# Optimization experiments

Measured on AMD Instinct MI355X. Metric: run time of the kernel, lower is better.

Reference implementation:

```python
import jax, jax.numpy as jnp
import numpy as np

T, D, H, O = 1048576, 64, 128, 32  # tokens, input_size, expert hidden, expert output_size


def setup_inputs() -> dict:
    key = jax.random.key(0)
    ks = jax.random.split(key, 11)
    s = 0.02
    return {
        "x": jax.random.normal(ks[0], (T, D), dtype=jnp.float32),
        "topk_idx": jax.random.randint(ks[1], (T, 2), 0, 2),
        "weights": jax.random.uniform(ks[2], (T, 2), dtype=jnp.float32),
        # expert 0: MLP D -> H -> O
        "W0a": jax.random.normal(ks[3], (D, H), dtype=jnp.float32) * s,
        "b0a": jnp.zeros((H,), dtype=jnp.float32),
        "W0b": jax.random.normal(ks[4], (H, O), dtype=jnp.float32) * s,
        "b0b": jnp.zeros((O,), dtype=jnp.float32),
        # expert 1: MLP (D + O) -> H -> O  (memory-enhanced input)
        "W1a": jax.random.normal(ks[5], (D + O, H), dtype=jnp.float32) * s,
        "b1a": jnp.zeros((H,), dtype=jnp.float32),
        "W1b": jax.random.normal(ks[6], (H, O), dtype=jnp.float32) * s,
        "b1b": jnp.zeros((O,), dtype=jnp.float32),
    }


def reference(x, topk_idx, weights, W0a, b0a, W0b, b0b, W1a, b1a, W1b, b1b):
    mask0 = (topk_idx == 0).any(axis=1)  # [T]
    mask1 = (topk_idx == 1).any(axis=1)  # [T]

    # expert 0 output, zero where not routed (matches zeros buffer + masked scatter)
    e0 = jnp.maximum(x @ W0a + b0a, 0.0) @ W0b + b0b      # [T, O]
    out0 = jnp.where(mask0[:, None], e0, 0.0)

    # last_valid_fill: forward-fill last valid row index (invalid -> 0, then cummax)
    t = jnp.arange(T)
    idx = jax.lax.cummax(jnp.where(mask0, t, 0))           # [T] int
    filled = out0[idx]                                     # [T, O] gather rows

    # expert 1 on [x, last_valid_out0], zero where not routed
    x1 = jnp.concatenate([x, filled], axis=1)              # [T, D+O]
    e1 = jnp.maximum(x1 @ W1a + b1a, 0.0) @ W1b + b1b      # [T, O]
    out1 = jnp.where(mask1[:, None], e1, 0.0)

    w = weights[:, :1]                                     # [T, 1]
    return w * out0 + (1.0 - w) * out1
```

## Files before the change

kernel.cpp:

```cpp
#include <hip/hip_runtime.h>
#include <hip/hip_bf16.h>

#define TROWS 1048576
#define RPB   256
#define NCHUNK (TROWS / RPB)
#define LSTRIDE 36

typedef float f32x4  __attribute__((ext_vector_type(4)));
typedef short bf16x8 __attribute__((ext_vector_type(8)));
typedef short bf16x4 __attribute__((ext_vector_type(4)));

#define MFMA(a, b, c) __builtin_amdgcn_mfma_f32_16x16x32_bf16(a, b, c, 0, 0, 0)

__device__ __forceinline__ short f2bf(float v) {
    __hip_bfloat16 b = __float2bfloat16(v);
    return __builtin_bit_cast(short, b);
}
__device__ __forceinline__ float bf2f(short s) {
    unsigned u = ((unsigned)(unsigned short)s) << 16;
    return __builtin_bit_cast(float, u);
}

__global__ __launch_bounds__(64) void prep_kernel(
    const float* __restrict__ W0a, const float* __restrict__ W0b,
    const float* __restrict__ W1a, const float* __restrict__ W1b,
    bf16x8* __restrict__ frag)
{
    const int fid = blockIdx.x, l = threadIdx.x, c = l & 15, g = l >> 4;
    const float* W; int N, ks, nt;
    if (fid < 16)      { W = W0a; N = 128; ks = fid >> 3;        nt = fid & 7; }
    else if (fid < 24) { W = W0b; N = 32;  ks = (fid - 16) >> 1; nt = (fid - 16) & 1; }
    else if (fid < 48) { W = W1a; N = 128; ks = (fid - 24) >> 3; nt = (fid - 24) & 7; }
    else               { W = W1b; N = 32;  ks = (fid - 48) >> 1; nt = (fid - 48) & 1; }
    bf16x8 f;
    #pragma unroll
    for (int j = 0; j < 8; ++j) {
        const int k = 32 * ks + ((j < 4) ? (4 * g + j) : (16 + 4 * g + (j - 4)));
        f[j] = f2bf(W[k * N + 16 * nt + c]);
    }
    frag[fid * 64 + l] = f;
}

__global__ __launch_bounds__(256) void fused_kernel(
    const float* __restrict__ x, const int* __restrict__ topk,
    const float* __restrict__ wts,
    const float* __restrict__ b0a, const float* __restrict__ b0b,
    const float* __restrict__ b1a, const float* __restrict__ b1b,
    const bf16x8* __restrict__ frag,
    float* __restrict__ out)
{
    const int b = blockIdx.x;
    const int tid = threadIdx.x, wv = tid >> 6, l = tid & 63, c = l & 15, g = l >> 4;

    __shared__ short out0_lds[257 * LSTRIDE];
    __shared__ int wtot[4];

    const int t = b * RPB + tid;
    const int2 tko = ((const int2*)topk)[t];
    const bool m0o = (tko.x == 0) || (tko.y == 0);
    int s = m0o ? t : 0;
    #pragma unroll
    for (int off = 1; off < 64; off <<= 1) {
        int u = __shfl_up(s, off, 64);
        if (l >= off) s = max(s, u);
    }
    if (l == 63) wtot[wv] = s;

    int p = 0;
    for (int base = b * RPB - 64; base >= 0; base -= 64) {
        const int2 tkq = ((const int2*)topk)[base + l];
        const bool mm = (tkq.x == 0) || (tkq.y == 0);
        const unsigned long long bal = __ballot(mm);
        if (bal) { p = base + 63 - __clzll(bal); break; }
    }
    const int2 tkp = ((const int2*)topk)[p];
    const bool m0p = (tkp.x == 0) || (tkp.y == 0);

    bf16x8 xf[4][2];
    #pragma unroll
    for (int rt = 0; rt < 4; ++rt) {
        const int row = b * RPB + wv * 64 + rt * 16 + c;
        const float* xr = x + (size_t)row * 64;
        #pragma unroll
        for (int ks = 0; ks < 2; ++ks) {
            f32x4 a  = *(const f32x4*)(xr + 32 * ks + 4 * g);
            f32x4 bb = *(const f32x4*)(xr + 32 * ks + 16 + 4 * g);
            #pragma unroll
            for (int j = 0; j < 4; ++j) { xf[rt][ks][j] = f2bf(a[j]); xf[rt][ks][4 + j] = f2bf(bb[j]); }
        }
    }
    bf16x8 xfp[2];
    {
        const float* xp = x + (size_t)p * 64;
        #pragma unroll
        for (int ks = 0; ks < 2; ++ks) {
            f32x4 a  = *(const f32x4*)(xp + 32 * ks + 4 * g);
            f32x4 bb = *(const f32x4*)(xp + 32 * ks + 16 + 4 * g);
            #pragma unroll
            for (int j = 0; j < 4; ++j) { xfp[ks][j] = f2bf(a[j]); xfp[ks][4 + j] = f2bf(bb[j]); }
        }
    }

    f32x4 acc2a[5][2];
    {
        f32x4 bi0 = *(const f32x4*)(b0b + 4 * g);
        f32x4 bi1 = *(const f32x4*)(b0b + 16 + 4 * g);
        #pragma unroll
        for (int rt = 0; rt < 5; ++rt) { acc2a[rt][0] = bi0; acc2a[rt][1] = bi1; }
    }
    #pragma unroll
    for (int k2 = 0; k2 < 4; ++k2) {
        bf16x8 fa[2][2];
        #pragma unroll
        for (int ks = 0; ks < 2; ++ks)
            #pragma unroll
            for (int ntl = 0; ntl < 2; ++ntl)
                fa[ks][ntl] = frag[(ks * 8 + 2 * k2 + ntl) * 64 + l];
        f32x4 bi[2];
        bi[0] = *(const f32x4*)(b0a + 16 * (2 * k2) + 4 * g);
        bi[1] = *(const f32x4*)(b0a + 16 * (2 * k2 + 1) + 4 * g);

        f32x4 a1[5][2];
        #pragma unroll
        for (int rt = 0; rt < 5; ++rt) { a1[rt][0] = bi[0]; a1[rt][1] = bi[1]; }
        #pragma unroll
        for (int rt = 0; rt < 5; ++rt)
            #pragma unroll
            for (int ks = 0; ks < 2; ++ks) {
                const bf16x8 xv = (rt < 4) ? xf[rt][ks] : xfp[ks];
                a1[rt][0] = MFMA(fa[ks][0], xv, a1[rt][0]);
                a1[rt][1] = MFMA(fa[ks][1], xv, a1[rt][1]);
            }

        bf16x8 fb[2];
        fb[0] = frag[(16 + k2 * 2 + 0) * 64 + l];
        fb[1] = frag[(16 + k2 * 2 + 1) * 64 + l];
        #pragma unroll
        for (int rt = 0; rt < 5; ++rt) {
            bf16x8 hf;
            #pragma unroll
            for (int j = 0; j < 8; ++j)
                hf[j] = f2bf(fmaxf(a1[rt][j >> 2][j & 3], 0.0f));
            acc2a[rt][0] = MFMA(fb[0], hf, acc2a[rt][0]);
            acc2a[rt][1] = MFMA(fb[1], hf, acc2a[rt][1]);
        }
    }

    #pragma unroll
    for (int rt = 0; rt < 4; ++rt) {
        const int slot = wv * 64 + rt * 16 + c;
        const int2 tk = ((const int2*)topk)[b * RPB + slot];
        const bool m0 = (tk.x == 0) || (tk.y == 0);
        #pragma unroll
        for (int ot = 0; ot < 2; ++ot) {
            bf16x4 v;
            #pragma unroll
            for (int j = 0; j < 4; ++j) v[j] = f2bf(m0 ? acc2a[rt][ot][j] : 0.0f);
            *(bf16x4*)(&out0_lds[slot * LSTRIDE + 16 * ot + 4 * g]) = v;
        }
    }
    if (wv == 0 && c == 0) {
        #pragma unroll
        for (int ot = 0; ot < 2; ++ot) {
            bf16x4 v;
            #pragma unroll
            for (int j = 0; j < 4; ++j) v[j] = f2bf(m0p ? acc2a[4][ot][j] : 0.0f);
            *(bf16x4*)(&out0_lds[256 * LSTRIDE + 16 * ot + 4 * g]) = v;
        }
    }

    __syncthreads();

    int pre = 0;
    #pragma unroll
    for (int w2 = 0; w2 < 4; ++w2)
        if (w2 < wv) pre = max(pre, wtot[w2]);
    const int s_full = max(pre, s);

    bf16x8 xf2[4];
    #pragma unroll
    for (int rt = 0; rt < 4; ++rt) {
        const int sF = __shfl(s_full, rt * 16 + c, 64);
        const int slot = (sF > 0) ? (sF - b * RPB) : 256;
        const short* fr = &out0_lds[slot * LSTRIDE];
        bf16x4 fa_ = *(const bf16x4*)(fr + 4 * g);
        bf16x4 fb_ = *(const bf16x4*)(fr + 16 + 4 * g);
        #pragma unroll
        for (int j = 0; j < 4; ++j) { xf2[rt][j] = fa_[j]; xf2[rt][4 + j] = fb_[j]; }
    }

    f32x4 acc2b[4][2];
    {
        f32x4 bi0 = *(const f32x4*)(b1b + 4 * g);
        f32x4 bi1 = *(const f32x4*)(b1b + 16 + 4 * g);
        #pragma unroll
        for (int rt = 0; rt < 4; ++rt) { acc2b[rt][0] = bi0; acc2b[rt][1] = bi1; }
    }
    #pragma unroll
    for (int k2 = 0; k2 < 4; ++k2) {
        bf16x8 fa[3][2];
        #pragma unroll
        for (int ks = 0; ks < 3; ++ks)
            #pragma unroll
            for (int ntl = 0; ntl < 2; ++ntl)
                fa[ks][ntl] = frag[(24 + ks * 8 + 2 * k2 + ntl) * 64 + l];
        f32x4 bi[2];
        bi[0] = *(const f32x4*)(b1a + 16 * (2 * k2) + 4 * g);
        bi[1] = *(const f32x4*)(b1a + 16 * (2 * k2 + 1) + 4 * g);

        f32x4 a1[4][2];
        #pragma unroll
        for (int rt = 0; rt < 4; ++rt) { a1[rt][0] = bi[0]; a1[rt][1] = bi[1]; }
        #pragma unroll
        for (int rt = 0; rt < 4; ++rt) {
            #pragma unroll
            for (int ks = 0; ks < 2; ++ks) {
                a1[rt][0] = MFMA(fa[ks][0], xf[rt][ks], a1[rt][0]);
                a1[rt][1] = MFMA(fa[ks][1], xf[rt][ks], a1[rt][1]);
            }
            a1[rt][0] = MFMA(fa[2][0], xf2[rt], a1[rt][0]);
            a1[rt][1] = MFMA(fa[2][1], xf2[rt], a1[rt][1]);
        }

        bf16x8 fb[2];
        fb[0] = frag[(48 + k2 * 2 + 0) * 64 + l];
        fb[1] = frag[(48 + k2 * 2 + 1) * 64 + l];
        #pragma unroll
        for (int rt = 0; rt < 4; ++rt) {
            bf16x8 hf;
            #pragma unroll
            for (int j = 0; j < 8; ++j)
                hf[j] = f2bf(fmaxf(a1[rt][j >> 2][j & 3], 0.0f));
            acc2b[rt][0] = MFMA(fb[0], hf, acc2b[rt][0]);
            acc2b[rt][1] = MFMA(fb[1], hf, acc2b[rt][1]);
        }
    }

    #pragma unroll
    for (int rt = 0; rt < 4; ++rt) {
        const int row = b * RPB + wv * 64 + rt * 16 + c;
        const int2 tk = ((const int2*)topk)[row];
        const bool m1 = (tk.x == 1) || (tk.y == 1);
        const float w  = wts[(size_t)row * 2];
        const float wc = 1.0f - w;
        const int oslot = wv * 64 + rt * 16 + c;
        #pragma unroll
        for (int ot = 0; ot < 2; ++ot) {
            bf16x4 oa = *(const bf16x4*)(&out0_lds[oslot * LSTRIDE + 16 * ot + 4 * g]);
            f32x4 r;
            #pragma unroll
            for (int j = 0; j < 4; ++j) {
                const float e1 = m1 ? acc2b[rt][ot][j] : 0.0f;
                r[j] = w * bf2f(oa[j]) + wc * e1;
            }
            *(f32x4*)(out + (size_t)row * 32 + 16 * ot + 4 * g) = r;
        }
    }
}

extern "C" void kernel_launch(void* const* d_in, const int* in_sizes, int n_in,
                              void* d_out, int out_size, void* d_ws, size_t ws_size,
                              hipStream_t stream)
{
    const float* x    = (const float*)d_in[0];
    const int*   topk = (const int*)  d_in[1];
    const float* wts  = (const float*)d_in[2];
    const float* W0a  = (const float*)d_in[3];
    const float* b0a  = (const float*)d_in[4];
    const float* W0b  = (const float*)d_in[5];
    const float* b0b  = (const float*)d_in[6];
    const float* W1a  = (const float*)d_in[7];
    const float* b1a  = (const float*)d_in[8];
    const float* W1b  = (const float*)d_in[9];
    const float* b1b  = (const float*)d_in[10];
    float* out = (float*)d_out;

    bf16x8* frag = (bf16x8*)d_ws;

    prep_kernel<<<dim3(56), dim3(64), 0, stream>>>(W0a, W0b, W1a, W1b, frag);
    fused_kernel<<<dim3(NCHUNK), dim3(RPB), 0, stream>>>(
        x, topk, wts, b0a, b0b, b1a, b1b, frag, out);
}
```

Baseline: 151.4 us.

## Stage weight fragments in LDS, restructure MLP loops, add occupancy hint

Each block now copies the expert-0 bf16 weight fragments into shared memory, then reloads the buffer with expert-1 fragments between phases. MFMA operands come from LDS instead of per-wave global loads. The first-layer loop now computes hidden activations one row tile at a time, which lowers live accumulator registers, and launch_bounds asks for 3 blocks per SIMD. The carry-in row's expert-0 output is computed only by wave 3 instead of as a fifth tile in every wave. The cost is about 32 KB of extra LDS per block, plus extra barriers and copy work that could limit occupancy.

```diff
diff --git a/kernel.cpp b/kernel.cpp
--- a/kernel.cpp
+++ b/kernel.cpp
@@ -41,7 +41,7 @@
     frag[fid * 64 + l] = f;
 }
 
-__global__ __launch_bounds__(256) void fused_kernel(
+__global__ __launch_bounds__(256, 3) void fused_kernel(
     const float* __restrict__ x, const int* __restrict__ topk,
     const float* __restrict__ wts,
     const float* __restrict__ b0a, const float* __restrict__ b0b,
@@ -50,12 +50,22 @@
     float* __restrict__ out)
 {
     const int b = blockIdx.x;
+    const int bb = b * RPB;
     const int tid = threadIdx.x, wv = tid >> 6, l = tid & 63, c = l & 15, g = l >> 4;
 
-    __shared__ short out0_lds[257 * LSTRIDE];
+    __shared__ __align__(16) short frag_lds[32 * 64 * 8];
+    __shared__ __align__(16) short out0_lds[257 * LSTRIDE];
     __shared__ int wtot[4];
 
-    const int t = b * RPB + tid;
+    #define LDSF(fl) (*(const bf16x8*)&frag_lds[(((fl) * 64) + l) * 8])
+
+    #pragma unroll
+    for (int i = 0; i < 6; ++i) {
+        const int e = tid + i * 256;
+        *(f32x4*)&frag_lds[e * 8] = *(const f32x4*)&frag[e];
+    }
+
+    const int t = bb + tid;
     const int2 tko = ((const int2*)topk)[t];
     const bool m0o = (tko.x == 0) || (tko.y == 0);
     int s = m0o ? t : 0;
@@ -67,7 +77,7 @@
     if (l == 63) wtot[wv] = s;
 
     int p = 0;
-    for (int base = b * RPB - 64; base >= 0; base -= 64) {
+    for (int base = bb - 64; base >= 0; base -= 64) {
         const int2 tkq = ((const int2*)topk)[base + l];
         const bool mm = (tkq.x == 0) || (tkq.y == 0);
         const unsigned long long bal = __ballot(mm);
@@ -79,77 +89,73 @@
     bf16x8 xf[4][2];
     #pragma unroll
     for (int rt = 0; rt < 4; ++rt) {
-        const int row = b * RPB + wv * 64 + rt * 16 + c;
+        const int row = bb + wv * 64 + rt * 16 + c;
         const float* xr = x + (size_t)row * 64;
         #pragma unroll
         for (int ks = 0; ks < 2; ++ks) {
             f32x4 a  = *(const f32x4*)(xr + 32 * ks + 4 * g);
-            f32x4 bb = *(const f32x4*)(xr + 32 * ks + 16 + 4 * g);
-            #pragma unroll
-            for (int j = 0; j < 4; ++j) { xf[rt][ks][j] = f2bf(a[j]); xf[rt][ks][4 + j] = f2bf(bb[j]); }
+            f32x4 b2 = *(const f32x4*)(xr + 32 * ks + 16 + 4 * g);
+            #pragma unroll
+            for (int j = 0; j < 4; ++j) { xf[rt][ks][j] = f2bf(a[j]); xf[rt][ks][4 + j] = f2bf(b2[j]); }
         }
     }
     bf16x8 xfp[2];
-    {
+    if (wv == 3) {
         const float* xp = x + (size_t)p * 64;
         #pragma unroll
         for (int ks = 0; ks < 2; ++ks) {
             f32x4 a  = *(const f32x4*)(xp + 32 * ks + 4 * g);
-            f32x4 bb = *(const f32x4*)(xp + 32 * ks + 16 + 4 * g);
-            #pragma unroll
-            for (int j = 0; j < 4; ++j) { xfp[ks][j] = f2bf(a[j]); xfp[ks][4 + j] = f2bf(bb[j]); }
-        }
-    }
-
-    f32x4 acc2a[5][2];
+            f32x4 b2 = *(const f32x4*)(xp + 32 * ks + 16 + 4 * g);
+            #pragma unroll
+            for (int j = 0; j < 4; ++j) { xfp[ks][j] = f2bf(a[j]); xfp[ks][4 + j] = f2bf(b2[j]); }
+        }
+    }
+
+    __syncthreads();
+
+    int pre = 0;
+    #pragma unroll
+    for (int w2 = 0; w2 < 4; ++w2)
+        if (w2 < wv) pre = max(pre, wtot[w2]);
+    const int s_full = max(pre, s);
+
+    f32x4 acc2a[4][2];
     {
         f32x4 bi0 = *(const f32x4*)(b0b + 4 * g);
         f32x4 bi1 = *(const f32x4*)(b0b + 16 + 4 * g);
         #pragma unroll
-        for (int rt = 0; rt < 5; ++rt) { acc2a[rt][0] = bi0; acc2a[rt][1] = bi1; }
+        for (int rt = 0; rt < 4; ++rt) { acc2a[rt][0] = bi0; acc2a[rt][1] = bi1; }
     }
     #pragma unroll
     for (int k2 = 0; k2 < 4; ++k2) {
-        bf16x8 fa[2][2];
-        #pragma unroll
-        for (int ks = 0; ks < 2; ++ks)
-            #pragma unroll
-            for (int ntl = 0; ntl < 2; ++ntl)
-                fa[ks][ntl] = frag[(ks * 8 + 2 * k2 + ntl) * 64 + l];
-        f32x4 bi[2];
-        bi[0] = *(const f32x4*)(b0a + 16 * (2 * k2) + 4 * g);
-        bi[1] = *(const f32x4*)(b0a + 16 * (2 * k2 + 1) + 4 * g);
-
-        f32x4 a1[5][2];
-        #pragma unroll
-        for (int rt = 0; rt < 5; ++rt) { a1[rt][0] = bi[0]; a1[rt][1] = bi[1]; }
-        #pragma unroll
-        for (int rt = 0; rt < 5; ++rt)
-            #pragma unroll
-            for (int ks = 0; ks < 2; ++ks) {
-                const bf16x8 xv = (rt < 4) ? xf[rt][ks] : xfp[ks];
-                a1[rt][0] = MFMA(fa[ks][0], xv, a1[rt][0]);
-                a1[rt][1] = MFMA(fa[ks][1], xv, a1[rt][1]);
-            }
-
-        bf16x8 fb[2];
-        fb[0] = frag[(16 + k2 * 2 + 0) * 64 + l];
-        fb[1] = frag[(16 + k2 * 2 + 1) * 64 + l];
-        #pragma unroll
-        for (int rt = 0; rt < 5; ++rt) {
+        const bf16x8 fa00 = LDSF(0 * 8 + 2 * k2 + 0);
+        const bf16x8 fa01 = LDSF(0 * 8 + 2 * k2 + 1);
+        const bf16x8 fa10 = LDSF(1 * 8 + 2 * k2 + 0);
+        const bf16x8 fa11 = LDSF(1 * 8 + 2 * k2 + 1);
+        const bf16x8 fb0  = LDSF(16 + 2 * k2 + 0);
+        const bf16x8 fb1  = LDSF(16 + 2 * k2 + 1);
+        const f32x4 bi0 = *(const f32x4*)(b0a + 16 * (2 * k2 + 0) + 4 * g);
+        const f32x4 bi1 = *(const f32x4*)(b0a + 16 * (2 * k2 + 1) + 4 * g);
+        #pragma unroll
+        for (int rt = 0; rt < 4; ++rt) {
+            f32x4 a10 = bi0, a11 = bi1;
+            a10 = MFMA(fa00, xf[rt][0], a10);
+            a10 = MFMA(fa10, xf[rt][1], a10);
+            a11 = MFMA(fa01, xf[rt][0], a11);
+            a11 = MFMA(fa11, xf[rt][1], a11);
             bf16x8 hf;
             #pragma unroll
             for (int j = 0; j < 8; ++j)
-                hf[j] = f2bf(fmaxf(a1[rt][j >> 2][j & 3], 0.0f));
-            acc2a[rt][0] = MFMA(fb[0], hf, acc2a[rt][0]);
-            acc2a[rt][1] = MFMA(fb[1], hf, acc2a[rt][1]);
+                hf[j] = f2bf(fmaxf((j < 4 ? a10 : a11)[j & 3], 0.0f));
+            acc2a[rt][0] = MFMA(fb0, hf, acc2a[rt][0]);
+            acc2a[rt][1] = MFMA(fb1, hf, acc2a[rt][1]);
         }
     }
 
     #pragma unroll
     for (int rt = 0; rt < 4; ++rt) {
         const int slot = wv * 64 + rt * 16 + c;
-        const int2 tk = ((const int2*)topk)[b * RPB + slot];
+        const int2 tk = ((const int2*)topk)[bb + slot];
         const bool m0 = (tk.x == 0) || (tk.y == 0);
         #pragma unroll
         for (int ot = 0; ot < 2; ++ot) {
@@ -159,29 +165,58 @@
             *(bf16x4*)(&out0_lds[slot * LSTRIDE + 16 * ot + 4 * g]) = v;
         }
     }
-    if (wv == 0 && c == 0) {
-        #pragma unroll
-        for (int ot = 0; ot < 2; ++ot) {
-            bf16x4 v;
-            #pragma unroll
-            for (int j = 0; j < 4; ++j) v[j] = f2bf(m0p ? acc2a[4][ot][j] : 0.0f);
-            *(bf16x4*)(&out0_lds[256 * LSTRIDE + 16 * ot + 4 * g]) = v;
+
+    if (wv == 3) {
+        f32x4 accp[2];
+        accp[0] = *(const f32x4*)(b0b + 4 * g);
+        accp[1] = *(const f32x4*)(b0b + 16 + 4 * g);
+        #pragma unroll
+        for (int k2 = 0; k2 < 4; ++k2) {
+            const bf16x8 fa00 = LDSF(0 * 8 + 2 * k2 + 0);
+            const bf16x8 fa01 = LDSF(0 * 8 + 2 * k2 + 1);
+            const bf16x8 fa10 = LDSF(1 * 8 + 2 * k2 + 0);
+            const bf16x8 fa11 = LDSF(1 * 8 + 2 * k2 + 1);
+            const bf16x8 fb0  = LDSF(16 + 2 * k2 + 0);
+            const bf16x8 fb1  = LDSF(16 + 2 * k2 + 1);
+            f32x4 a10 = *(const f32x4*)(b0a + 16 * (2 * k2 + 0) + 4 * g);
+            f32x4 a11 = *(const f32x4*)(b0a + 16 * (2 * k2 + 1) + 4 * g);
+            a10 = MFMA(fa00, xfp[0], a10);
+            a10 = MFMA(fa10, xfp[1], a10);
+            a11 = MFMA(fa01, xfp[0], a11);
+            a11 = MFMA(fa11, xfp[1], a11);
+            bf16x8 hf;
+            #pragma unroll
+            for (int j = 0; j < 8; ++j)
+                hf[j] = f2bf(fmaxf((j < 4 ? a10 : a11)[j & 3], 0.0f));
+            accp[0] = MFMA(fb0, hf, accp[0]);
+            accp[1] = MFMA(fb1, hf, accp[1]);
+        }
+        if (c == 0) {
+            #pragma unroll
+            for (int ot = 0; ot < 2; ++ot) {
+                bf16x4 v;
+                #pragma unroll
+                for (int j = 0; j < 4; ++j) v[j] = f2bf(m0p ? accp[ot][j] : 0.0f);
+                *(bf16x4*)(&out0_lds[256 * LSTRIDE + 16 * ot + 4 * g]) = v;
+            }
         }
     }
 
     __syncthreads();
 
-    int pre = 0;
-    #pragma unroll
-    for (int w2 = 0; w2 < 4; ++w2)
-        if (w2 < wv) pre = max(pre, wtot[w2]);
-    const int s_full = max(pre, s);
+    #pragma unroll
+    for (int i = 0; i < 8; ++i) {
+        const int e = tid + i * 256;
+        *(f32x4*)&frag_lds[e * 8] = *(const f32x4*)&frag[24 * 64 + e];
+    }
+
+    __syncthreads();
 
     bf16x8 xf2[4];
     #pragma unroll
     for (int rt = 0; rt < 4; ++rt) {
         const int sF = __shfl(s_full, rt * 16 + c, 64);
-        const int slot = (sF > 0) ? (sF - b * RPB) : 256;
+        const int slot = (sF > 0) ? (sF - bb) : 256;
         const short* fr = &out0_lds[slot * LSTRIDE];
         bf16x4 fa_ = *(const bf16x4*)(fr + 4 * g);
         bf16x4 fb_ = *(const bf16x4*)(fr + 16 + 4 * g);
@@ -198,55 +233,45 @@
     }
     #pragma unroll
     for (int k2 = 0; k2 < 4; ++k2) {
-        bf16x8 fa[3][2];
-        #pragma unroll
-        for (int ks = 0; ks < 3; ++ks)
-            #pragma unroll
-            for (int ntl = 0; ntl < 2; ++ntl)
-                fa[ks][ntl] = frag[(24 + ks * 8 + 2 * k2 + ntl) * 64 + l];
-        f32x4 bi[2];
-        bi[0] = *(const f32x4*)(b1a + 16 * (2 * k2) + 4 * g);
-        bi[1] = *(const f32x4*)(b1a + 16 * (2 * k2 + 1) + 4 * g);
-
-        f32x4 a1[4][2];
-        #pragma unroll
-        for (int rt = 0; rt < 4; ++rt) { a1[rt][0] = bi[0]; a1[rt][1] = bi[1]; }
+        const bf16x8 fa00 = LDSF(0 * 8 + 2 * k2 + 0);
+        const bf16x8 fa01 = LDSF(0 * 8 + 2 * k2 + 1);
+        const bf16x8 fa10 = LDSF(1 * 8 + 2 * k2 + 0);
+        const bf16x8 fa11 = LDSF(1 * 8 + 2 * k2 + 1);
+        const bf16x8 fa20 = LDSF(2 * 8 + 2 * k2 + 0);
+        const bf16x8 fa21 = LDSF(2 * 8 + 2 * k2 + 1);
+        const bf16x8 fb0  = LDSF(24 + 2 * k2 + 0);
+        const bf16x8 fb1  = LDSF(24 + 2 * k2 + 1);
+        const f32x4 bi0 = *(const f32x4*)(b1a + 16 * (2 * k2 + 0) + 4 * g);
+        const f32x4 bi1 = *(const f32x4*)(b1a + 16 * (2 * k2 + 1) + 4 * g);
         #pragma unroll
         for (int rt = 0; rt < 4; ++rt) {
-            #pragma unroll
-            for (int ks = 0; ks < 2; ++ks) {
-                a1[rt][0] = MFMA(fa[ks][0], xf[rt][ks], a1[rt][0]);
-                a1[rt][1] = MFMA(fa[ks][1], xf[rt][ks], a1[rt][1]);
-            }
-            a1[rt][0] = MFMA(fa[2][0], xf2[rt], a1[rt][0]);
-            a1[rt][1] = MFMA(fa[2][1], xf2[rt], a1[rt][1]);
-        }
-
-        bf16x8 fb[2];
-        fb[0] = frag[(48 + k2 * 2 + 0) * 64 + l];
-        fb[1] = frag[(48 + k2 * 2 + 1) * 64 + l];
-        #pragma unroll
-        for (int rt = 0; rt < 4; ++rt) {
+            f32x4 a10 = bi0, a11 = bi1;
+            a10 = MFMA(fa00, xf[rt][0], a10);
+            a10 = MFMA(fa10, xf[rt][1], a10);
+            a10 = MFMA(fa20, xf2[rt], a10);
+            a11 = MFMA(fa01, xf[rt][0], a11);
+            a11 = MFMA(fa11, xf[rt][1], a11);
+            a11 = MFMA(fa21, xf2[rt], a11);
             bf16x8 hf;
             #pragma unroll
             for (int j = 0; j < 8; ++j)
-                hf[j] = f2bf(fmaxf(a1[rt][j >> 2][j & 3], 0.0f));
-            acc2b[rt][0] = MFMA(fb[0], hf, acc2b[rt][0]);
-            acc2b[rt][1] = MFMA(fb[1], hf, acc2b[rt][1]);
+                hf[j] = f2bf(fmaxf((j < 4 ? a10 : a11)[j & 3], 0.0f));
+            acc2b[rt][0] = MFMA(fb0, hf, acc2b[rt][0]);
+            acc2b[rt][1] = MFMA(fb1, hf, acc2b[rt][1]);
         }
     }
 
     #pragma unroll
     for (int rt = 0; rt < 4; ++rt) {
-        const int row = b * RPB + wv * 64 + rt * 16 + c;
+        const int slot = wv * 64 + rt * 16 + c;
+        const int row = bb + slot;
         const int2 tk = ((const int2*)topk)[row];
         const bool m1 = (tk.x == 1) || (tk.y == 1);
         const float w  = wts[(size_t)row * 2];
         const float wc = 1.0f - w;
-        const int oslot = wv * 64 + rt * 16 + c;
         #pragma unroll
         for (int ot = 0; ot < 2; ++ot) {
-            bf16x4 oa = *(const bf16x4*)(&out0_lds[oslot * LSTRIDE + 16 * ot + 4 * g]);
+            bf16x4 oa = *(const bf16x4*)(&out0_lds[slot * LSTRIDE + 16 * ot + 4 * g]);
             f32x4 r;
             #pragma unroll
             for (int j = 0; j < 4; ++j) {
@@ -256,6 +281,7 @@
             *(f32x4*)(out + (size_t)row * 32 + 16 * ot + 4 * g) = r;
         }
     }
+    #undef LDSF
 }
 
 extern "C" void kernel_launch(void* const* d_in, const int* in_sizes, int n_in,
@@ -278,6 +304,6 @@
     bf16x8* frag = (bf16x8*)d_ws;
 
     prep_kernel<<<dim3(56), dim3(64), 0, stream>>>(W0a, W0b, W1a, W1b, frag);
-    fused_kernel<<<dim3(NCHUNK), dim3(RPB), 0, stream>>>(
+    fused_kernel<<<dim3(NCHUNK), dim3(256), 0, stream>>>(
         x, topk, wts, b0a, b0b, b1a, b1b, frag, out);
 }
```

New measurement: 122.9 us. 18.8% less time.
